# Kernel optimization log

Hardware: AMD Instinct MI355X
Metric: run time of the kernel (lower is better)

## Reference

```python
import jax, jax.numpy as jnp
import numpy as np
import math

B, C, S, O, K = 64, 271, 512, 512, 32  # seq_len S must equal out_channels O (einsum constraint in original)

def setup_inputs() -> dict:
    key = jax.random.key(0)
    k1, k2, k3, k4, k5 = jax.random.split(key, 5)
    x = jax.random.normal(k1, (B, C, S), dtype=jnp.float32)
    fourier_features = jax.random.normal(k2, (O, K, K, 4), dtype=jnp.float32)
    sensor_positions = jax.random.uniform(k3, (C, 2), dtype=jnp.float32)
    proj_w = jax.random.normal(k4, (O, C), dtype=jnp.float32) / np.float32(math.sqrt(C))
    proj_b = jax.random.normal(k5, (O,), dtype=jnp.float32) * 0.02
    return {"x": x, "fourier_features": fourier_features,
            "sensor_positions": sensor_positions, "proj_w": proj_w, "proj_b": proj_b}

def reference(x, fourier_features, sensor_positions, proj_w, proj_b):
    Kdim = fourier_features.shape[1]
    freqs = 2.0 * jnp.pi * jnp.arange(Kdim, dtype=jnp.float32) / Kdim
    # meshgrid(freqs_x, freqs_y, indexing='ij') stacked on last dim -> [K,K,2]
    grid = jnp.stack(jnp.meshgrid(freqs, freqs, indexing='ij'), axis=-1)
    # feature map is batch-independent: [C,K,K,2] -> sin/cos cat -> [C,K,K,4]
    fm = sensor_positions[:, None, None, :] * grid[None]
    fm = jnp.concatenate([jnp.sin(fm), jnp.cos(fm)], axis=-1)
    # attention logits [O,C]; original expands over batch but result is identical per batch
    att = jnp.einsum('ckhw,okhw->oc', fm, fourier_features)
    att = jax.nn.softmax(att, axis=0)  # softmax over out_channels (dim=1 of [B,O,C])
    # 1x1 Conv1d: [B,C,S] -> [B,O,S]
    xp = jnp.einsum('bcs,oc->bos', x, proj_w) + proj_b[None, :, None]
    # original: einsum('bci,bio->bco', xp[B,O,S], attn[B,O,C]); contraction over S(==O)
    out = jnp.einsum('bps,sq->bpq', xp, att)  # [B,O,C]
    return out
```

## Files before the change

### kernel.cpp

```cpp
#include <hip/hip_runtime.h>
#include <hip/hip_bf16.h>
#include <math.h>


typedef short s16x8 __attribute__((ext_vector_type(8)));
typedef short s16x4 __attribute__((ext_vector_type(4)));
typedef float f32x4 __attribute__((ext_vector_type(4)));

#define GLOBAL_AS __attribute__((address_space(1)))
#define LDS_AS    __attribute__((address_space(3)))

__device__ __forceinline__ short f2bf(float f) {
    __hip_bfloat16 h = __float2bfloat16(f);
    return *reinterpret_cast<short*>(&h);
}

#define Cdim 271
#define CpK  288
#define Sdim 512
#define Odim 512
#define MF   17344
#define MFp  17408

template<int MODE, int SWAP, int AF32>
__global__ __launch_bounds__(512) void gemm_bf16(
    const void* __restrict__ Av, int lda,
    const short* __restrict__ BT, int ldb,
    int nk,
    void* __restrict__ OutV,
    const float* __restrict__ bias)
{
    const int m0 = (SWAP ? blockIdx.x : blockIdx.y) * 128;
    const int n0 = (SWAP ? blockIdx.y : blockIdx.x) * 128;

    __shared__ short pool[24576];

    const int t = threadIdx.x;
    const int lane = t & 63;
    const int wid = t >> 6;
    const int wr = wid >> 2;
    const int wc = wid & 3;
    const int lr = lane & 15, lkq = lane >> 4;

    f32x4 acc[4][2];
    #pragma unroll
    for (int i = 0; i < 4; ++i)
        #pragma unroll
        for (int j = 0; j < 2; ++j)
            acc[i][j] = (f32x4){0.f, 0.f, 0.f, 0.f};

    const int srowB = wid * 16 + (lane >> 2);
    const int skk   = (((lane & 3) ^ ((lane >> 3) & 3)) * 8);
    const short* pB = BT + (long)(n0 + srowB) * ldb + skk;
    const int ldsOff = wid * 512;

    const short* pA_bf = (const short*)Av + (long)(m0 + srowB) * lda + skk;
    const int arow = t >> 2;
    const int aslot = t & 3;
    const int afc = (aslot ^ ((arow >> 1) & 3)) * 8;
    const int agrow = (m0 + arow < MF) ? (m0 + arow) : (MF - 1);
    const float* pA_f32 = (const float*)Av + (long)agrow * lda + afc;
    const int aWr = arow * 32 + aslot * 8;

    const int kxs = ((lkq ^ ((lr >> 1) & 3)) << 3);
    const int aBase = (wr * 64 + lr) * 32 + kxs;
    const int bBase = (wc * 32 + lr) * 32 + kxs;

    auto stageB = [&](int buf, int kt) {
        __builtin_amdgcn_global_load_lds((const GLOBAL_AS void*)(pB + kt * 32),
            (LDS_AS void*)&pool[12288 + buf * 4096 + ldsOff], 16, 0, 0);
    };
    auto stageA_bf = [&](int buf, int kt) {
        __builtin_amdgcn_global_load_lds((const GLOBAL_AS void*)(pA_bf + kt * 32),
            (LDS_AS void*)&pool[buf * 4096 + ldsOff], 16, 0, 0);
    };

    auto compute = [&](int buf) {
        s16x8 af[4], bfv[2];
        #pragma unroll
        for (int m = 0; m < 4; ++m)
            af[m] = *(const s16x8*)&pool[buf * 4096 + aBase + m * 512];
        #pragma unroll
        for (int n = 0; n < 2; ++n)
            bfv[n] = *(const s16x8*)&pool[12288 + buf * 4096 + bBase + n * 512];
        #pragma unroll
        for (int m = 0; m < 4; ++m)
            #pragma unroll
            for (int n = 0; n < 2; ++n)
                acc[m][n] = __builtin_amdgcn_mfma_f32_16x16x32_bf16(af[m], bfv[n], acc[m][n], 0, 0, 0);
    };

    if (AF32) {
        f32x4 aP0, aP1, aN0, aN1;
        auto loadA = [&](int kt, f32x4& v0, f32x4& v1) {
            const float* p = pA_f32 + kt * 32;
            v0 = *(const f32x4 GLOBAL_AS*)(p);
            v1 = *(const f32x4 GLOBAL_AS*)(p + 4);
        };
        auto writeA = [&](int buf, const f32x4& v0, const f32x4& v1) {
            s16x8 w;
            #pragma unroll
            for (int j = 0; j < 4; ++j) { w[j] = f2bf(v0[j]); w[4 + j] = f2bf(v1[j]); }
            *(s16x8*)&pool[buf * 4096 + aWr] = w;
        };
        loadA(0, aP0, aP1); stageB(0, 0);
        writeA(0, aP0, aP1);
        loadA(1, aP0, aP1); stageB(1, 1);
        int bc = 0, bs = 2;
        for (int kt = 0; kt < nk; ++kt) {
            if (kt + 1 < nk) asm volatile("s_waitcnt vmcnt(3) lgkmcnt(0)" ::: "memory");
            else             asm volatile("s_waitcnt vmcnt(0) lgkmcnt(0)" ::: "memory");
            __builtin_amdgcn_s_barrier();
            __builtin_amdgcn_sched_barrier(0);
            if (kt + 2 < nk) { loadA(kt + 2, aN0, aN1); stageB(bs, kt + 2); }
            compute(bc);
            if (kt + 1 < nk) writeA((bc == 2) ? 0 : bc + 1, aP0, aP1);
            aP0 = aN0; aP1 = aN1;
            bc = (bc == 2) ? 0 : bc + 1;
            bs = (bs == 2) ? 0 : bs + 1;
        }
    } else {
        stageA_bf(0, 0); stageB(0, 0);
        stageA_bf(1, 1); stageB(1, 1);
        int bc = 0, bs = 2;
        for (int kt = 0; kt < nk; ++kt) {
            if (kt + 1 < nk) asm volatile("s_waitcnt vmcnt(2)" ::: "memory");
            else             asm volatile("s_waitcnt vmcnt(0)" ::: "memory");
            __builtin_amdgcn_s_barrier();
            __builtin_amdgcn_sched_barrier(0);
            if (kt + 2 < nk) { stageA_bf(bs, kt + 2); stageB(bs, kt + 2); }
            compute(bc);
            bc = (bc == 2) ? 0 : bc + 1;
            bs = (bs == 2) ? 0 : bs + 1;
        }
    }

    if (MODE == 0) {
        __syncthreads();
        short* T = pool;
        #pragma unroll
        for (int i = 0; i < 4; ++i) {
            const int ml = wr * 64 + i * 16 + lkq * 4;
            #pragma unroll
            for (int j = 0; j < 2; ++j) {
                const int ql = wc * 32 + j * 16 + lr;
                s16x4 v;
                #pragma unroll
                for (int r = 0; r < 4; ++r) v[r] = f2bf(acc[i][j][r]);
                *(s16x4*)&T[ql * 132 + ml] = v;
            }
        }
        __syncthreads();
        short* Oy = (short*)OutV;
        #pragma unroll
        for (int p = 0; p < 4; ++p) {
            const int ql = p * 32 + (t >> 4);
            const int gq = n0 + ql;
            const int mlc = (t & 15) * 8;
            const s16x8 v = *(const s16x8*)&T[ql * 132 + mlc];
            const int gm0 = m0 + mlc;
            if (gq < Cdim && gm0 < MF) {
                const int b0 = gm0 / Cdim;
                const int c0 = gm0 - b0 * Cdim;
                if (c0 + 8 <= Cdim) {
                    *(s16x8*)&Oy[((long)b0 * Cdim + gq) * CpK + c0] = v;
                } else {
                    #pragma unroll
                    for (int r = 0; r < 8; ++r) {
                        const int gm = gm0 + r;
                        if (gm < MF) {
                            const int bb = gm / Cdim;
                            const int cc = gm - bb * Cdim;
                            Oy[((long)bb * Cdim + gq) * CpK + cc] = v[r];
                        }
                    }
                }
            }
        }
    } else {
        float* O = (float*)OutV;
        #pragma unroll
        for (int j = 0; j < 2; ++j) {
            const int gn = n0 + wc * 32 + j * 16 + lr;
            if (gn >= MF) continue;
            const int b = gn / Cdim;
            const int q = gn - b * Cdim;
            float* ob = O + (long)b * Odim * Cdim + q;
            #pragma unroll
            for (int i = 0; i < 4; ++i) {
                const int gmb = m0 + wr * 64 + i * 16 + lkq * 4;
                #pragma unroll
                for (int r = 0; r < 4; ++r) {
                    const int gm = gmb + r;
                    ob[(long)gm * Cdim] = acc[i][j][r] + bias[gm];
                }
            }
        }
    }
}

__global__ __launch_bounds__(256) void ff_reduce(const float* __restrict__ ff,
                                                 float* __restrict__ GT)
{
    __shared__ float L[2][32 * 132];
    const int t = threadIdx.x;
    const int half = t >> 7;
    const int tl = t & 127;
    const int o = blockIdx.x * 2 + half;
    const float* base = ff + (long)o * 4096;
    #pragma unroll
    for (int ch = 0; ch < 8; ++ch) {
        const int g = ch * 512 + tl * 4;
        const f32x4 v = *(const f32x4*)&base[g];
        *(f32x4*)&L[half][(g >> 7) * 132 + (g & 127)] = v;
    }
    __syncthreads();
    const int gq = tl >> 5, idx = tl & 31;
    float s = 0.f;
    if (gq == 0 || gq == 2) {
        const int w = (gq == 0) ? 0 : 2;
        #pragma unroll 8
        for (int j = 0; j < 32; ++j) s += L[half][idx * 132 + j * 4 + w];
    } else {
        const int w = (gq == 1) ? 1 : 3;
        #pragma unroll 8
        for (int i = 0; i < 32; ++i) s += L[half][i * 132 + idx * 4 + w];
    }
    GT[tl * 512 + o] = s;
}

__device__ __forceinline__ float wave_max(float v) {
    #pragma unroll
    for (int off = 32; off; off >>= 1) v = fmaxf(v, __shfl_xor(v, off));
    return v;
}
__device__ __forceinline__ float wave_sum(float v) {
    #pragma unroll
    for (int off = 32; off; off >>= 1) v += __shfl_xor(v, off);
    return v;
}

__global__ __launch_bounds__(256) void att_fused(
    const float* __restrict__ GT,
    const float* __restrict__ sp,
    short* __restrict__ attT,
    const float* __restrict__ pw,
    short* __restrict__ pwb)
{
    const int c = blockIdx.x;
    const int t = threadIdx.x;
    short* row = attT + (long)c * Sdim;
    if (c >= Cdim) {
        row[t] = 0; row[t + 256] = 0;
        const int bi = c - Cdim;
        if (bi < 72) {
            const int idx8 = (bi * 256 + t) * 8;
            const int p = idx8 / CpK;
            const int k0 = idx8 - p * CpK;
            s16x8 v;
            #pragma unroll
            for (int r = 0; r < 8; ++r) {
                const int k = k0 + r;
                v[r] = (k < Cdim) ? f2bf(pw[(long)p * Cdim + k]) : (short)0;
            }
            *(s16x8*)&pwb[idx8] = v;
        }
        return;
    }
    __shared__ float u[128];
    __shared__ float red[4];
    if (t < 128) {
        const int g = t >> 5, k = t & 31;
        const float f = 6.283185307179586477f * (float)k / 32.0f;
        const float p = sp[c * 2 + (g & 1)];
        const float ang = p * f;
        u[t] = (g < 2) ? sinf(ang) : cosf(ang);
    }
    __syncthreads();

    float l0 = 0.f, l1 = 0.f;
    #pragma unroll 8
    for (int k = 0; k < 128; ++k) {
        const float uk = u[k];
        l0 = fmaf(GT[k * 512 + t], uk, l0);
        l1 = fmaf(GT[k * 512 + t + 256], uk, l1);
    }

    const int lane = t & 63, wid = t >> 6;
    float m = wave_max(fmaxf(l0, l1));
    if (lane == 0) red[wid] = m;
    __syncthreads();
    m = fmaxf(fmaxf(red[0], red[1]), fmaxf(red[2], red[3]));
    const float e0 = expf(l0 - m), e1 = expf(l1 - m);
    float s = wave_sum(e0 + e1);
    __syncthreads();
    if (lane == 0) red[wid] = s;
    __syncthreads();
    s = red[0] + red[1] + red[2] + red[3];
    const float inv = 1.f / s;
    row[t]       = f2bf(e0 * inv);
    row[t + 256] = f2bf(e1 * inv);
}

extern "C" void kernel_launch(void* const* d_in, const int* in_sizes, int n_in,
                              void* d_out, int out_size, void* d_ws, size_t ws_size,
                              hipStream_t stream)
{
    const float* x  = (const float*)d_in[0];
    const float* ff = (const float*)d_in[1];
    const float* sp = (const float*)d_in[2];
    const float* pw = (const float*)d_in[3];
    const float* pb = (const float*)d_in[4];
    float* out = (float*)d_out;

    const int S = Sdim, O = Odim;

    float* ws   = (float*)d_ws;
    float* GT   = ws;
    short* attT = (short*)(GT + 128 * 512);
    short* pwb  = attT + 384L * S;
    short* yT   = pwb + (long)O * CpK;

    ff_reduce<<<256, 256, 0, stream>>>(ff, GT);

    att_fused<<<384, 256, 0, stream>>>(GT, sp, attT, pw, pwb);

    gemm_bf16<0, 1, 1><<<dim3(MFp / 128, 3), 512, 0, stream>>>(
        (const void*)x, S, attT, S, S / 32, (void*)yT, nullptr);

    gemm_bf16<1, 0, 0><<<dim3(MFp / 128, O / 128), 512, 0, stream>>>(
        (const void*)pwb, CpK, yT, CpK, CpK / 32, (void*)out, pb);
}
```

Baseline: 57.95 us.

## Restructure first GEMM to full-N 64-row tiles and batch softmax rows per block

Replaces the templated GEMM with two specialised kernels. The first GEMM now uses 64-row M tiles that each cover all 384 attention columns, so each tile of x is read and converted to bf16 once instead of once per N tile. It uses register-staged double buffering in place of the previous triple-buffered async loads. The attention kernel now computes four softmax rows per 512-thread block, reusing each GT load across four channels. The pw conversion is folded into fewer blocks, and the zero-padding writes for attT rows 271-383 are dropped, which assumes those workspace rows are already zero.

```diff
diff --git a/kernel.cpp b/kernel.cpp
--- a/kernel.cpp
+++ b/kernel.cpp
@@ -22,17 +22,138 @@
 #define MF   17344
 #define MFp  17408
 
-template<int MODE, int SWAP, int AF32>
-__global__ __launch_bounds__(512) void gemm_bf16(
-    const void* __restrict__ Av, int lda,
-    const short* __restrict__ BT, int ldb,
-    int nk,
-    void* __restrict__ OutV,
+__global__ __launch_bounds__(512, 4) void gemm7(
+    const float* __restrict__ x, const short* __restrict__ attT,
+    short* __restrict__ yT)
+{
+    const int m0 = blockIdx.x * 64;
+    __shared__ short pool[28672];
+
+    const int t = threadIdx.x;
+    const int lane = t & 63;
+    const int wid = t >> 6;
+    const int lr = lane & 15, lkq = lane >> 4;
+
+    f32x4 acc[4][3];
+    #pragma unroll
+    for (int i = 0; i < 4; ++i)
+        #pragma unroll
+        for (int j = 0; j < 3; ++j)
+            acc[i][j] = (f32x4){0.f, 0.f, 0.f, 0.f};
+
+    const int ar = t >> 3, as_ = t & 7;
+    const int ag = (as_ >> 1) ^ ((ar >> 1) & 3);
+    const int agrow = (m0 + ar < MF) ? (m0 + ar) : (MF - 1);
+    const float* pA = x + (long)agrow * Sdim + ag * 8 + (as_ & 1) * 4;
+    const int aWr = ar * 32 + as_ * 4;
+
+    const int brow_ = t >> 2;
+    const int bs_ = t & 3;
+    const int bg = bs_ ^ ((t >> 3) & 3);
+
+    const int kxs = ((lkq ^ ((lr >> 1) & 3)) << 3);
+
+    f32x4 aR;
+    s16x8 bR0, bR1, bR2;
+
+    auto loadA = [&](int kt) { aR = *(const f32x4*)(pA + kt * 32); };
+    auto loadB = [&](int kt) {
+        bR0 = *(const s16x8*)&attT[(long)(brow_)*Sdim + kt * 32 + bg * 8];
+        bR1 = *(const s16x8*)&attT[(long)(128 + brow_) * Sdim + kt * 32 + bg * 8];
+        bR2 = *(const s16x8*)&attT[(long)(256 + brow_) * Sdim + kt * 32 + bg * 8];
+    };
+    auto writeA = [&](int buf) {
+        s16x4 w;
+        #pragma unroll
+        for (int j = 0; j < 4; ++j) w[j] = f2bf(aR[j]);
+        *(s16x4*)&pool[buf * 2048 + aWr] = w;
+    };
+    auto writeB = [&](int buf) {
+        short* bb = &pool[4096 + buf * 12288];
+        *(s16x8*)&bb[(brow_) * 32 + bs_ * 8] = bR0;
+        *(s16x8*)&bb[(128 + brow_) * 32 + bs_ * 8] = bR1;
+        *(s16x8*)&bb[(256 + brow_) * 32 + bs_ * 8] = bR2;
+    };
+    auto compute = [&](int buf) {
+        s16x8 af[4];
+        #pragma unroll
+        for (int m = 0; m < 4; ++m)
+            af[m] = *(const s16x8*)&pool[buf * 2048 + (m * 16 + lr) * 32 + kxs];
+        #pragma unroll
+        for (int n3 = 0; n3 < 3; ++n3) {
+            const s16x8 bf_ = *(const s16x8*)&pool[4096 + buf * 12288 +
+                (wid * 48 + n3 * 16 + lr) * 32 + kxs];
+            #pragma unroll
+            for (int m = 0; m < 4; ++m)
+                acc[m][n3] = __builtin_amdgcn_mfma_f32_16x16x32_bf16(af[m], bf_, acc[m][n3], 0, 0, 0);
+        }
+    };
+
+    const int nk = Sdim / 32;
+    loadA(0); loadB(0);
+    writeA(0); writeB(0);
+    loadA(1); loadB(1);
+    int buf = 0;
+    for (int kt = 0; kt < nk; ++kt) {
+        asm volatile("s_waitcnt lgkmcnt(0)" ::: "memory");
+        __builtin_amdgcn_s_barrier();
+        __builtin_amdgcn_sched_barrier(0);
+        if (kt + 1 < nk) {
+            writeA(buf ^ 1); writeB(buf ^ 1);
+            if (kt + 2 < nk) { loadA(kt + 2); loadB(kt + 2); }
+        }
+        compute(buf);
+        buf ^= 1;
+    }
+
+    __syncthreads();
+    short* T = pool;
+    #pragma unroll
+    for (int i = 0; i < 4; ++i) {
+        const int ml = i * 16 + lkq * 4;
+        #pragma unroll
+        for (int n3 = 0; n3 < 3; ++n3) {
+            const int ql = wid * 48 + n3 * 16 + lr;
+            s16x4 v;
+            #pragma unroll
+            for (int r = 0; r < 4; ++r) v[r] = f2bf(acc[i][n3][r]);
+            *(s16x4*)&T[ql * 68 + ml] = v;
+        }
+    }
+    __syncthreads();
+    #pragma unroll
+    for (int p = 0; p < 6; ++p) {
+        const int gq = p * 64 + (t >> 3);
+        const int mlc = (t & 7) * 8;
+        const int gm0 = m0 + mlc;
+        if (gq >= Cdim || gm0 >= MF) continue;
+        const s16x8 v = *(const s16x8*)&T[gq * 68 + mlc];
+        const int b0 = gm0 / Cdim;
+        const int c0 = gm0 - b0 * Cdim;
+        if (c0 + 8 <= Cdim) {
+            *(s16x8*)&yT[((long)b0 * Cdim + gq) * CpK + c0] = v;
+        } else {
+            #pragma unroll
+            for (int r = 0; r < 8; ++r) {
+                const int gm = gm0 + r;
+                if (gm < MF) {
+                    const int bb = gm / Cdim;
+                    const int cc = gm - bb * Cdim;
+                    yT[((long)bb * Cdim + gq) * CpK + cc] = v[r];
+                }
+            }
+        }
+    }
+}
+
+__global__ __launch_bounds__(512) void gemm8k(
+    const short* __restrict__ A,
+    const short* __restrict__ BT,
+    float* __restrict__ O,
     const float* __restrict__ bias)
 {
-    const int m0 = (SWAP ? blockIdx.x : blockIdx.y) * 128;
-    const int n0 = (SWAP ? blockIdx.y : blockIdx.x) * 128;
-
+    const int m0 = blockIdx.y * 128;
+    const int n0 = blockIdx.x * 128;
     __shared__ short pool[24576];
 
     const int t = threadIdx.x;
@@ -49,32 +170,22 @@
         for (int j = 0; j < 2; ++j)
             acc[i][j] = (f32x4){0.f, 0.f, 0.f, 0.f};
 
-    const int srowB = wid * 16 + (lane >> 2);
-    const int skk   = (((lane & 3) ^ ((lane >> 3) & 3)) * 8);
-    const short* pB = BT + (long)(n0 + srowB) * ldb + skk;
+    const int srow = wid * 16 + (lane >> 2);
+    const int skk  = (((lane & 3) ^ ((lane >> 3) & 3)) * 8);
+    const short* pA = A + (long)(m0 + srow) * CpK + skk;
+    const short* pB = BT + (long)(n0 + srow) * CpK + skk;
     const int ldsOff = wid * 512;
-
-    const short* pA_bf = (const short*)Av + (long)(m0 + srowB) * lda + skk;
-    const int arow = t >> 2;
-    const int aslot = t & 3;
-    const int afc = (aslot ^ ((arow >> 1) & 3)) * 8;
-    const int agrow = (m0 + arow < MF) ? (m0 + arow) : (MF - 1);
-    const float* pA_f32 = (const float*)Av + (long)agrow * lda + afc;
-    const int aWr = arow * 32 + aslot * 8;
 
     const int kxs = ((lkq ^ ((lr >> 1) & 3)) << 3);
     const int aBase = (wr * 64 + lr) * 32 + kxs;
     const int bBase = (wc * 32 + lr) * 32 + kxs;
 
-    auto stageB = [&](int buf, int kt) {
+    auto stage = [&](int buf, int kt) {
+        __builtin_amdgcn_global_load_lds((const GLOBAL_AS void*)(pA + kt * 32),
+            (LDS_AS void*)&pool[buf * 4096 + ldsOff], 16, 0, 0);
         __builtin_amdgcn_global_load_lds((const GLOBAL_AS void*)(pB + kt * 32),
             (LDS_AS void*)&pool[12288 + buf * 4096 + ldsOff], 16, 0, 0);
     };
-    auto stageA_bf = [&](int buf, int kt) {
-        __builtin_amdgcn_global_load_lds((const GLOBAL_AS void*)(pA_bf + kt * 32),
-            (LDS_AS void*)&pool[buf * 4096 + ldsOff], 16, 0, 0);
-    };
-
     auto compute = [&](int buf) {
         s16x8 af[4], bfv[2];
         #pragma unroll
@@ -90,110 +201,34 @@
                 acc[m][n] = __builtin_amdgcn_mfma_f32_16x16x32_bf16(af[m], bfv[n], acc[m][n], 0, 0, 0);
     };
 
-    if (AF32) {
-        f32x4 aP0, aP1, aN0, aN1;
-        auto loadA = [&](int kt, f32x4& v0, f32x4& v1) {
-            const float* p = pA_f32 + kt * 32;
-            v0 = *(const f32x4 GLOBAL_AS*)(p);
-            v1 = *(const f32x4 GLOBAL_AS*)(p + 4);
-        };
-        auto writeA = [&](int buf, const f32x4& v0, const f32x4& v1) {
-            s16x8 w;
-            #pragma unroll
-            for (int j = 0; j < 4; ++j) { w[j] = f2bf(v0[j]); w[4 + j] = f2bf(v1[j]); }
-            *(s16x8*)&pool[buf * 4096 + aWr] = w;
-        };
-        loadA(0, aP0, aP1); stageB(0, 0);
-        writeA(0, aP0, aP1);
-        loadA(1, aP0, aP1); stageB(1, 1);
-        int bc = 0, bs = 2;
-        for (int kt = 0; kt < nk; ++kt) {
-            if (kt + 1 < nk) asm volatile("s_waitcnt vmcnt(3) lgkmcnt(0)" ::: "memory");
-            else             asm volatile("s_waitcnt vmcnt(0) lgkmcnt(0)" ::: "memory");
-            __builtin_amdgcn_s_barrier();
-            __builtin_amdgcn_sched_barrier(0);
-            if (kt + 2 < nk) { loadA(kt + 2, aN0, aN1); stageB(bs, kt + 2); }
-            compute(bc);
-            if (kt + 1 < nk) writeA((bc == 2) ? 0 : bc + 1, aP0, aP1);
-            aP0 = aN0; aP1 = aN1;
-            bc = (bc == 2) ? 0 : bc + 1;
-            bs = (bs == 2) ? 0 : bs + 1;
-        }
-    } else {
-        stageA_bf(0, 0); stageB(0, 0);
-        stageA_bf(1, 1); stageB(1, 1);
-        int bc = 0, bs = 2;
-        for (int kt = 0; kt < nk; ++kt) {
-            if (kt + 1 < nk) asm volatile("s_waitcnt vmcnt(2)" ::: "memory");
-            else             asm volatile("s_waitcnt vmcnt(0)" ::: "memory");
-            __builtin_amdgcn_s_barrier();
-            __builtin_amdgcn_sched_barrier(0);
-            if (kt + 2 < nk) { stageA_bf(bs, kt + 2); stageB(bs, kt + 2); }
-            compute(bc);
-            bc = (bc == 2) ? 0 : bc + 1;
-            bs = (bs == 2) ? 0 : bs + 1;
-        }
-    }
-
-    if (MODE == 0) {
-        __syncthreads();
-        short* T = pool;
+    const int nk = CpK / 32;
+    stage(0, 0); stage(1, 1);
+    int bc = 0, bs = 2;
+    for (int kt = 0; kt < nk; ++kt) {
+        if (kt + 1 < nk) asm volatile("s_waitcnt vmcnt(2)" ::: "memory");
+        else             asm volatile("s_waitcnt vmcnt(0)" ::: "memory");
+        __builtin_amdgcn_s_barrier();
+        __builtin_amdgcn_sched_barrier(0);
+        if (kt + 2 < nk) stage(bs, kt + 2);
+        compute(bc);
+        bc = (bc == 2) ? 0 : bc + 1;
+        bs = (bs == 2) ? 0 : bs + 1;
+    }
+
+    #pragma unroll
+    for (int j = 0; j < 2; ++j) {
+        const int gn = n0 + wc * 32 + j * 16 + lr;
+        if (gn >= MF) continue;
+        const int b = gn / Cdim;
+        const int q = gn - b * Cdim;
+        float* ob = O + (long)b * Odim * Cdim + q;
         #pragma unroll
         for (int i = 0; i < 4; ++i) {
-            const int ml = wr * 64 + i * 16 + lkq * 4;
-            #pragma unroll
-            for (int j = 0; j < 2; ++j) {
-                const int ql = wc * 32 + j * 16 + lr;
-                s16x4 v;
-                #pragma unroll
-                for (int r = 0; r < 4; ++r) v[r] = f2bf(acc[i][j][r]);
-                *(s16x4*)&T[ql * 132 + ml] = v;
-            }
-        }
-        __syncthreads();
-        short* Oy = (short*)OutV;
-        #pragma unroll
-        for (int p = 0; p < 4; ++p) {
-            const int ql = p * 32 + (t >> 4);
-            const int gq = n0 + ql;
-            const int mlc = (t & 15) * 8;
-            const s16x8 v = *(const s16x8*)&T[ql * 132 + mlc];
-            const int gm0 = m0 + mlc;
-            if (gq < Cdim && gm0 < MF) {
-                const int b0 = gm0 / Cdim;
-                const int c0 = gm0 - b0 * Cdim;
-                if (c0 + 8 <= Cdim) {
-                    *(s16x8*)&Oy[((long)b0 * Cdim + gq) * CpK + c0] = v;
-                } else {
-                    #pragma unroll
-                    for (int r = 0; r < 8; ++r) {
-                        const int gm = gm0 + r;
-                        if (gm < MF) {
-                            const int bb = gm / Cdim;
-                            const int cc = gm - bb * Cdim;
-                            Oy[((long)bb * Cdim + gq) * CpK + cc] = v[r];
-                        }
-                    }
-                }
-            }
-        }
-    } else {
-        float* O = (float*)OutV;
-        #pragma unroll
-        for (int j = 0; j < 2; ++j) {
-            const int gn = n0 + wc * 32 + j * 16 + lr;
-            if (gn >= MF) continue;
-            const int b = gn / Cdim;
-            const int q = gn - b * Cdim;
-            float* ob = O + (long)b * Odim * Cdim + q;
-            #pragma unroll
-            for (int i = 0; i < 4; ++i) {
-                const int gmb = m0 + wr * 64 + i * 16 + lkq * 4;
-                #pragma unroll
-                for (int r = 0; r < 4; ++r) {
-                    const int gm = gmb + r;
-                    ob[(long)gm * Cdim] = acc[i][j][r] + bias[gm];
-                }
+            const int gmb = m0 + wr * 64 + i * 16 + lkq * 4;
+            #pragma unroll
+            for (int r = 0; r < 4; ++r) {
+                const int gm = gmb + r;
+                ob[(long)gm * Cdim] = acc[i][j][r] + bias[gm];
             }
         }
     }
@@ -240,66 +275,85 @@
     return v;
 }
 
-__global__ __launch_bounds__(256) void att_fused(
+__global__ __launch_bounds__(512) void att4(
     const float* __restrict__ GT,
     const float* __restrict__ sp,
     short* __restrict__ attT,
     const float* __restrict__ pw,
     short* __restrict__ pwb)
 {
-    const int c = blockIdx.x;
+    const int blk = blockIdx.x;
     const int t = threadIdx.x;
-    short* row = attT + (long)c * Sdim;
-    if (c >= Cdim) {
-        row[t] = 0; row[t + 256] = 0;
-        const int bi = c - Cdim;
-        if (bi < 72) {
-            const int idx8 = (bi * 256 + t) * 8;
-            const int p = idx8 / CpK;
-            const int k0 = idx8 - p * CpK;
-            s16x8 v;
-            #pragma unroll
-            for (int r = 0; r < 8; ++r) {
-                const int k = k0 + r;
-                v[r] = (k < Cdim) ? f2bf(pw[(long)p * Cdim + k]) : (short)0;
-            }
-            *(s16x8*)&pwb[idx8] = v;
-        }
+    if (blk >= 68) {
+        const int bi = blk - 68;
+        const int idx8 = (bi * 512 + t) * 8;
+        const int p = idx8 / CpK;
+        const int k0 = idx8 - p * CpK;
+        s16x8 v;
+        #pragma unroll
+        for (int r = 0; r < 8; ++r) {
+            const int k = k0 + r;
+            v[r] = (k < Cdim) ? f2bf(pw[(long)p * Cdim + k]) : (short)0;
+        }
+        *(s16x8*)&pwb[idx8] = v;
         return;
     }
-    __shared__ float u[128];
-    __shared__ float red[4];
-    if (t < 128) {
-        const int g = t >> 5, k = t & 31;
-        const float f = 6.283185307179586477f * (float)k / 32.0f;
-        const float p = sp[c * 2 + (g & 1)];
+
+    const int c0 = blk * 4;
+    __shared__ float u[4][128];
+    __shared__ float red[32];
+    {
+        const int ci = t >> 7, k = t & 127;
+        const int csafe = (c0 + ci < Cdim) ? (c0 + ci) : (Cdim - 1);
+        const int g = k >> 5, kk = k & 31;
+        const float f = 6.283185307179586477f * (float)kk / 32.0f;
+        const float p = sp[csafe * 2 + (g & 1)];
         const float ang = p * f;
-        u[t] = (g < 2) ? sinf(ang) : cosf(ang);
-    }
-    __syncthreads();
-
-    float l0 = 0.f, l1 = 0.f;
+        u[ci][k] = (g < 2) ? sinf(ang) : cosf(ang);
+    }
+    __syncthreads();
+
+    float l[4] = {0.f, 0.f, 0.f, 0.f};
     #pragma unroll 8
     for (int k = 0; k < 128; ++k) {
-        const float uk = u[k];
-        l0 = fmaf(GT[k * 512 + t], uk, l0);
-        l1 = fmaf(GT[k * 512 + t + 256], uk, l1);
+        const float g = GT[k * 512 + t];
+        #pragma unroll
+        for (int ci = 0; ci < 4; ++ci) l[ci] = fmaf(g, u[ci][k], l[ci]);
     }
 
     const int lane = t & 63, wid = t >> 6;
-    float m = wave_max(fmaxf(l0, l1));
-    if (lane == 0) red[wid] = m;
-    __syncthreads();
-    m = fmaxf(fmaxf(red[0], red[1]), fmaxf(red[2], red[3]));
-    const float e0 = expf(l0 - m), e1 = expf(l1 - m);
-    float s = wave_sum(e0 + e1);
-    __syncthreads();
-    if (lane == 0) red[wid] = s;
-    __syncthreads();
-    s = red[0] + red[1] + red[2] + red[3];
-    const float inv = 1.f / s;
-    row[t]       = f2bf(e0 * inv);
-    row[t + 256] = f2bf(e1 * inv);
+    float m[4];
+    #pragma unroll
+    for (int ci = 0; ci < 4; ++ci) m[ci] = wave_max(l[ci]);
+    if (lane == 0) {
+        #pragma unroll
+        for (int ci = 0; ci < 4; ++ci) red[wid * 4 + ci] = m[ci];
+    }
+    __syncthreads();
+    #pragma unroll
+    for (int ci = 0; ci < 4; ++ci) {
+        float mm = red[ci];
+        #pragma unroll
+        for (int w = 1; w < 8; ++w) mm = fmaxf(mm, red[w * 4 + ci]);
+        m[ci] = mm;
+    }
+    __syncthreads();
+    float e[4], s[4];
+    #pragma unroll
+    for (int ci = 0; ci < 4; ++ci) { e[ci] = expf(l[ci] - m[ci]); s[ci] = wave_sum(e[ci]); }
+    if (lane == 0) {
+        #pragma unroll
+        for (int ci = 0; ci < 4; ++ci) red[wid * 4 + ci] = s[ci];
+    }
+    __syncthreads();
+    #pragma unroll
+    for (int ci = 0; ci < 4; ++ci) {
+        float ss = red[ci];
+        #pragma unroll
+        for (int w = 1; w < 8; ++w) ss += red[w * 4 + ci];
+        const int c = c0 + ci;
+        if (c < Cdim) attT[(long)c * Sdim + t] = f2bf(e[ci] / ss);
+    }
 }
 
 extern "C" void kernel_launch(void* const* d_in, const int* in_sizes, int n_in,
@@ -313,21 +367,14 @@
     const float* pb = (const float*)d_in[4];
     float* out = (float*)d_out;
 
-    const int S = Sdim, O = Odim;
-
     float* ws   = (float*)d_ws;
     float* GT   = ws;
     short* attT = (short*)(GT + 128 * 512);
-    short* pwb  = attT + 384L * S;
-    short* yT   = pwb + (long)O * CpK;
+    short* pwb  = attT + 384L * Sdim;
+    short* yT   = pwb + (long)Odim * CpK;
 
     ff_reduce<<<256, 256, 0, stream>>>(ff, GT);
-
-    att_fused<<<384, 256, 0, stream>>>(GT, sp, attT, pw, pwb);
-
-    gemm_bf16<0, 1, 1><<<dim3(MFp / 128, 3), 512, 0, stream>>>(
-        (const void*)x, S, attT, S, S / 32, (void*)yT, nullptr);
-
-    gemm_bf16<1, 0, 0><<<dim3(MFp / 128, O / 128), 512, 0, stream>>>(
-        (const void*)pwb, CpK, yT, CpK, CpK / 32, (void*)out, pb);
-}
+    att4<<<104, 512, 0, stream>>>(GT, sp, attT, pw, pwb);
+    gemm7<<<MFp / 64, 512, 0, stream>>>(x, attT, yT);
+    gemm8k<<<dim3(MFp / 128, Odim / 128), 512, 0, stream>>>(pwb, yT, out, pb);
+}
```

New measurement: 63.50 us. 9.6% more time.
